# Kernel optimization log

Measured on AMD Instinct MI355X. Metric: run time of the kernel, lower is better.

## Reference

```python
import jax, jax.numpy as jnp
import numpy as np

B, L, DM, DI, N = 8, 2048, 512, 768, 8  # batch, seq, d_model, d_inner=int(1.5*512), d_state


def setup_inputs() -> dict:
    key = jax.random.key(0)
    ks = jax.random.split(key, 8)
    g = lambda k, shape, sc=1.0: (jax.random.normal(k, shape, jnp.float32) * sc)
    return {
        "x": g(ks[0], (B, L, DM)),
        "W_in": g(ks[1], (DM, 2 * DI), 0.02),    # in_proj weight (stored in->out)
        "A_log": g(ks[2], (DI, N)),               # nn.Parameter(randn)
        "D_param": g(ks[3], (DI,)),               # skip-connection D
        "W_x": g(ks[4], (DI, N), 0.02),           # x_proj weight
        "W_dt": g(ks[5], (N, DI), 0.02),          # dt_proj weight
        "b_dt": jnp.zeros((DI,), jnp.float32),    # dt_proj bias
        "W_out": g(ks[6], (DI, DM), 0.02),        # out_proj weight
    }


def reference(x, W_in, A_log, D_param, W_x, W_dt, b_dt, W_out):
    xz = x @ W_in                                  # (B,L,2*DI)
    d_inner = W_in.shape[1] // 2
    x_ssm, z = xz[..., :d_inner], xz[..., d_inner:]
    x_ssm = jax.nn.silu(x_ssm)                     # (B,L,DI)
    A = -jnp.exp(A_log.astype(jnp.float32))        # (DI,N)
    delta = jax.nn.softplus((x_ssm @ W_x) @ W_dt + b_dt)  # (B,L,DI)

    n_state = A.shape[-1]

    def step(h, inp):
        xt, dt = inp                               # each (B,DI)
        dA = jnp.exp(dt[..., None] * A)            # (B,DI,N)
        h = dA * h + dt[..., None] * xt[..., None]
        y = jnp.sum(h, axis=-1) + D_param * xt     # (B,DI)
        return h, y

    h0 = jnp.zeros((x.shape[0], d_inner, n_state), x_ssm.dtype)
    xs = (jnp.swapaxes(x_ssm, 0, 1), jnp.swapaxes(delta, 0, 1))  # (L,B,DI)
    _, ys = jax.lax.scan(step, h0, xs)             # ys: (L,B,DI)
    y = jnp.swapaxes(ys, 0, 1)                     # (B,L,DI)
    y = y * jax.nn.silu(z)
    return y @ W_out                               # (B,L,DM)
```

## Files before the change

### kernel.cpp

```cpp
#include <hip/hip_runtime.h>

typedef unsigned short bfu;
typedef __attribute__((ext_vector_type(8))) short short8;
typedef __attribute__((ext_vector_type(4))) float f32x4;

__device__ __forceinline__ float bf2f(bfu u){
  union { unsigned int i; float f; } v; v.i = ((unsigned int)u) << 16; return v.f;
}
__device__ __forceinline__ bfu f2bf(float f){
  union { float f; unsigned int i; } v; v.f = f;
  unsigned int r = (v.i + 0x7FFFu + ((v.i >> 16) & 1u)) >> 16;
  return (bfu)r;
}
__device__ __forceinline__ float fexp2(float x){ return __builtin_amdgcn_exp2f(x); }
__device__ __forceinline__ float flog2(float x){ return __builtin_amdgcn_logf(x); }
__device__ __forceinline__ float softplusf(float x){
  float t = fexp2(-fabsf(x) * 1.44269504088896f);
  return fmaxf(x, 0.f) + 0.69314718055995f * flog2(1.f + t);
}
__device__ __forceinline__ void gload16(const bfu* g, bfu* l){
  __builtin_amdgcn_global_load_lds((const __attribute__((address_space(1))) unsigned int*)g,
                                   (__attribute__((address_space(3))) unsigned int*)l, 16, 0, 0);
}

__global__ __launch_bounds__(256) void cvt_all_kernel(const float* __restrict__ x, bfu* __restrict__ x_bf,
                                                      const float* __restrict__ W_in, const float* __restrict__ W_out,
                                                      const float* __restrict__ W_x,
                                                      bfu* __restrict__ WinT, bfu* __restrict__ WoutT,
                                                      float* __restrict__ WxT){
  int g = blockIdx.x * 256 + threadIdx.x;
  if (g < 2097152){
    float4 v = ((const float4*)x)[g];
    ushort4 o;
    o.x = f2bf(v.x); o.y = f2bf(v.y); o.z = f2bf(v.z); o.w = f2bf(v.w);
    ((ushort4*)x_bf)[g] = o;
    return;
  }
  int h = g - 2097152;
  if (h < 786432){
    int r = h % 512, c = h / 512;
    WinT[h] = f2bf(W_in[(size_t)r * 1536 + c]);
  } else if (h < 786432 + 393216){
    int h2 = h - 786432;
    int r = h2 % 768, c = h2 / 768;
    WoutT[h2] = f2bf(W_out[(size_t)r * 512 + c]);
  } else if (h < 786432 + 393216 + 6144){
    int h2 = h - (786432 + 393216);
    int n = h2 / 768, k = h2 % 768;
    WxT[h2] = W_x[(size_t)k * 8 + n];
  }
}

template<int EPI, int KK>
__global__ __launch_bounds__(256)
void gemm_db(const bfu* __restrict__ Amat, const bfu* __restrict__ Bt,
             void* __restrict__ out0, void* __restrict__ out1,
             int NBN, int N)
{
  constexpr int NT = KK / 64;
  __shared__ bfu As[2 * 128 * 64];
  __shared__ bfu Bs[2 * 128 * 64];
  const int tid  = threadIdx.x;
  const int lane = tid & 63;
  const int w    = tid >> 6;
  const int wr   = w >> 1, wc = w & 1;

  const int cpx = gridDim.x >> 3;
  const int id  = blockIdx.x;
  const int nid = (id & 7) * cpx + (id >> 3);
  const int bn  = nid % NBN;
  const int bm  = nid / NBN;

  const int srow = tid >> 3;
  const int scol = ((tid & 7) ^ (srow & 7)) * 8;
  const bfu* gA = Amat + ((size_t)(bm * 128 + srow)) * KK + scol;
  const bfu* gB = Bt   + ((size_t)(bn * 128 + srow)) * KK + scol;
  bfu* lA = As + tid * 8;
  bfu* lB = Bs + tid * 8;

  auto STAGE = [&](int t, int sel){
    const int k0 = t * 64;
    #pragma unroll
    for (int i = 0; i < 4; i++){
      gload16(gA + (size_t)(i * 32) * KK + k0, lA + sel * 8192 + i * 2048);
      gload16(gB + (size_t)(i * 32) * KK + k0, lB + sel * 8192 + i * 2048);
    }
  };

  f32x4 acc[4][4];
  #pragma unroll
  for (int i = 0; i < 4; i++)
    #pragma unroll
    for (int j = 0; j < 4; j++)
      #pragma unroll
      for (int r = 0; r < 4; r++) acc[i][j][r] = 0.f;

  STAGE(0, 0);
  STAGE(1, 1);

  #pragma unroll
  for (int t = 0; t < NT; ++t){
    if (t + 1 < NT) asm volatile("s_waitcnt vmcnt(8)" ::: "memory");
    else            asm volatile("s_waitcnt vmcnt(0)" ::: "memory");
    __builtin_amdgcn_s_barrier();

    const bfu* Ab = As + (t & 1) * 8192;
    const bfu* Bb = Bs + (t & 1) * 8192;
    #pragma unroll
    for (int kk = 0; kk < 2; kk++){
      short8 a[4], b[4];
      const int sA = ((kk * 4 + (lane >> 4)) ^ (lane & 7)) * 8;
      #pragma unroll
      for (int m = 0; m < 4; m++){
        int r = wr * 64 + m * 16 + (lane & 15);
        a[m] = *(const short8*)&Ab[r * 64 + sA];
      }
      #pragma unroll
      for (int n = 0; n < 4; n++){
        int r = wc * 64 + n * 16 + (lane & 15);
        b[n] = *(const short8*)&Bb[r * 64 + sA];
      }
      __builtin_amdgcn_s_setprio(1);
      #pragma unroll
      for (int m = 0; m < 4; m++)
        #pragma unroll
        for (int n = 0; n < 4; n++)
          acc[m][n] = __builtin_amdgcn_mfma_f32_16x16x32_bf16(a[m], b[n], acc[m][n], 0, 0, 0);
      __builtin_amdgcn_s_setprio(0);
    }
    __builtin_amdgcn_s_barrier();
    if (t + 2 < NT) STAGE(t + 2, t & 1);
  }

  #pragma unroll
  for (int m = 0; m < 4; m++){
    #pragma unroll
    for (int n = 0; n < 4; n++){
      const int row0 = bm * 128 + wr * 64 + m * 16 + (lane >> 4) * 4;
      const int col  = bn * 128 + wc * 64 + n * 16 + (lane & 15);
      #pragma unroll
      for (int r = 0; r < 4; r++){
        float v = acc[m][n][r];
        int row = row0 + r;
        if (EPI == 0){
          float s = v / (1.f + __expf(-v));
          if (col < 768) ((bfu*)out0)[(size_t)row * 768 + col]         = f2bf(s);
          else           ((bfu*)out1)[(size_t)row * 768 + (col - 768)] = f2bf(s);
        } else {
          ((float*)out0)[(size_t)row * N + col] = v;
        }
      }
    }
  }
}

__global__ __launch_bounds__(256) void u_kernel(const bfu* __restrict__ xssm, const float* __restrict__ WxT,
                                                float* __restrict__ u){
  int wid = threadIdx.x >> 6, lane = threadIdx.x & 63;
  int row = blockIdx.x * 4 + wid;
  const bfu* xr = xssm + (size_t)row * 768;
  float acc[8];
  #pragma unroll
  for (int n = 0; n < 8; n++) acc[n] = 0.f;
  #pragma unroll
  for (int i = 0; i < 3; i++){
    int kb = i * 256 + lane * 4;
    ushort4 xq = *(const ushort4*)(xr + kb);
    float x0 = bf2f(xq.x), x1 = bf2f(xq.y), x2 = bf2f(xq.z), x3 = bf2f(xq.w);
    #pragma unroll
    for (int n = 0; n < 8; n++){
      float4 wv = *(const float4*)(WxT + (size_t)n * 768 + kb);
      acc[n] += x0 * wv.x + x1 * wv.y + x2 * wv.z + x3 * wv.w;
    }
  }
  #pragma unroll
  for (int n = 0; n < 8; n++){
    #pragma unroll
    for (int off = 32; off >= 1; off >>= 1) acc[n] += __shfl_xor(acc[n], off, 64);
  }
  if (lane == 0){
    float4 o0 = { acc[0], acc[1], acc[2], acc[3] };
    float4 o1 = { acc[4], acc[5], acc[6], acc[7] };
    *(float4*)(u + (size_t)row * 8)     = o0;
    *(float4*)(u + (size_t)row * 8 + 4) = o1;
  }
}

__global__ __launch_bounds__(128) void scan_phase1(const bfu* __restrict__ xssm, const float* __restrict__ u,
    const float* __restrict__ Wdt, const float* __restrict__ bdt, const float* __restrict__ A_log,
    float* __restrict__ Pws, float* __restrict__ Hws){
  int tid = threadIdx.x;
  int bid = blockIdx.x;
  int b = bid / 192; int rem = bid % 192;
  int c = rem / 3;   int dblk = rem % 3;
  int d0 = dblk * 256 + tid * 2;
  float Al2[2][8], H[2][8], Wr[2][8], bd[2], S[2];
  #pragma unroll
  for (int j = 0; j < 2; j++){
    bd[j] = bdt[d0 + j];
    S[j] = 0.f;
    #pragma unroll
    for (int n = 0; n < 8; n++){
      Al2[j][n] = -__expf(A_log[(size_t)(d0 + j) * 8 + n]) * 1.4426950408889634f;
      Wr[j][n]  = Wdt[(size_t)n * 768 + d0 + j];
      H[j][n] = 0.f;
    }
  }
  int r0 = b * 2048 + c * 32;
  size_t base = (size_t)r0 * 768 + d0;
  #pragma unroll 8
  for (int i = 0; i < 32; i++){
    float4 u0 = *(const float4*)(u + (size_t)(r0 + i) * 8);
    float4 u1 = *(const float4*)(u + (size_t)(r0 + i) * 8 + 4);
    ushort2 xq = *(const ushort2*)(xssm + base + (size_t)i * 768);
    #pragma unroll
    for (int j = 0; j < 2; j++){
      float xt = bf2f(j == 0 ? xq.x : xq.y);
      float dv = bd[j] + u0.x * Wr[j][0] + u0.y * Wr[j][1] + u0.z * Wr[j][2] + u0.w * Wr[j][3]
                       + u1.x * Wr[j][4] + u1.y * Wr[j][5] + u1.z * Wr[j][6] + u1.w * Wr[j][7];
      float dt = softplusf(dv);
      float dx = dt * xt;
      S[j] += dt;
      #pragma unroll
      for (int n = 0; n < 8; n++){
        float e = fexp2(dt * Al2[j][n]);
        H[j][n] = e * H[j][n] + dx;
      }
    }
  }
  size_t o = (((size_t)b * 64 + c) * 768 + d0) * 8;
  #pragma unroll
  for (int j = 0; j < 2; j++){
    float4 p0, p1;
    p0.x = fexp2(S[j] * Al2[j][0]); p0.y = fexp2(S[j] * Al2[j][1]);
    p0.z = fexp2(S[j] * Al2[j][2]); p0.w = fexp2(S[j] * Al2[j][3]);
    p1.x = fexp2(S[j] * Al2[j][4]); p1.y = fexp2(S[j] * Al2[j][5]);
    p1.z = fexp2(S[j] * Al2[j][6]); p1.w = fexp2(S[j] * Al2[j][7]);
    float4 h0 = { H[j][0], H[j][1], H[j][2], H[j][3] };
    float4 h1 = { H[j][4], H[j][5], H[j][6], H[j][7] };
    *(float4*)(Pws + o + j * 8)     = p0;
    *(float4*)(Pws + o + j * 8 + 4) = p1;
    *(float4*)(Hws + o + j * 8)     = h0;
    *(float4*)(Hws + o + j * 8 + 4) = h1;
  }
}

__global__ __launch_bounds__(256) void scan_phase2(float* __restrict__ Pws, const float* __restrict__ Hws){
  int g = blockIdx.x * 256 + threadIdx.x;
  int within = g % 6144;
  int b = g / 6144;
  size_t base = (size_t)b * 64 * 6144 + within;
  float hin = 0.f;
  #pragma unroll 8
  for (int c = 0; c < 64; c++){
    size_t idx = base + (size_t)c * 6144;
    float p = Pws[idx], hh = Hws[idx];
    Pws[idx] = hin;
    hin = p * hin + hh;
  }
}

__global__ __launch_bounds__(128) void scan_phase3(const bfu* __restrict__ xssm, const float* __restrict__ u,
    const float* __restrict__ Wdt, const float* __restrict__ bdt, const float* __restrict__ A_log,
    const float* __restrict__ Dp, const bfu* __restrict__ siluz, const float* __restrict__ Hin,
    bfu* __restrict__ yz){
  int tid = threadIdx.x;
  int bid = blockIdx.x;
  int b = bid / 192; int rem = bid % 192;
  int c = rem / 3;   int dblk = rem % 3;
  int d0 = dblk * 256 + tid * 2;
  float Al2[2][8], H[2][8], Wr[2][8], bd[2], Dd[2];
  size_t o = (((size_t)b * 64 + c) * 768 + d0) * 8;
  #pragma unroll
  for (int j = 0; j < 2; j++){
    bd[j] = bdt[d0 + j];
    Dd[j] = Dp[d0 + j];
    float4 h0 = *(const float4*)(Hin + o + j * 8);
    float4 h1 = *(const float4*)(Hin + o + j * 8 + 4);
    H[j][0] = h0.x; H[j][1] = h0.y; H[j][2] = h0.z; H[j][3] = h0.w;
    H[j][4] = h1.x; H[j][5] = h1.y; H[j][6] = h1.z; H[j][7] = h1.w;
    #pragma unroll
    for (int n = 0; n < 8; n++){
      Al2[j][n] = -__expf(A_log[(size_t)(d0 + j) * 8 + n]) * 1.4426950408889634f;
      Wr[j][n]  = Wdt[(size_t)n * 768 + d0 + j];
    }
  }
  int r0 = b * 2048 + c * 32;
  size_t base = (size_t)r0 * 768 + d0;
  #pragma unroll 8
  for (int i = 0; i < 32; i++){
    float4 u0 = *(const float4*)(u + (size_t)(r0 + i) * 8);
    float4 u1 = *(const float4*)(u + (size_t)(r0 + i) * 8 + 4);
    ushort2 xq = *(const ushort2*)(xssm + base + (size_t)i * 768);
    ushort2 zq = *(const ushort2*)(siluz + base + (size_t)i * 768);
    ushort2 oq;
    #pragma unroll
    for (int j = 0; j < 2; j++){
      float xt = bf2f(j == 0 ? xq.x : xq.y);
      float dv = bd[j] + u0.x * Wr[j][0] + u0.y * Wr[j][1] + u0.z * Wr[j][2] + u0.w * Wr[j][3]
                       + u1.x * Wr[j][4] + u1.y * Wr[j][5] + u1.z * Wr[j][6] + u1.w * Wr[j][7];
      float dt = softplusf(dv);
      float dx = dt * xt;
      float y = Dd[j] * xt;
      #pragma unroll
      for (int n = 0; n < 8; n++){
        float e = fexp2(dt * Al2[j][n]);
        H[j][n] = e * H[j][n] + dx;
        y += H[j][n];
      }
      float sz = bf2f(j == 0 ? zq.x : zq.y);
      bfu r = f2bf(y * sz);
      if (j == 0) oq.x = r; else oq.y = r;
    }
    *(ushort2*)(yz + base + (size_t)i * 768) = oq;
  }
}

extern "C" void kernel_launch(void* const* d_in, const int* in_sizes, int n_in,
                              void* d_out, int out_size, void* d_ws, size_t ws_size,
                              hipStream_t stream){
  const float* x     = (const float*)d_in[0];
  const float* W_in  = (const float*)d_in[1];
  const float* A_log = (const float*)d_in[2];
  const float* D_par = (const float*)d_in[3];
  const float* W_x   = (const float*)d_in[4];
  const float* W_dt  = (const float*)d_in[5];
  const float* b_dt  = (const float*)d_in[6];
  const float* W_out = (const float*)d_in[7];
  float* out = (float*)d_out;
  (void)in_sizes; (void)n_in; (void)out_size; (void)ws_size;

  char* base = (char*)d_ws;
  size_t off = 0;
  auto alloc = [&](size_t bytes)->char*{
    char* p = base + off; off += (bytes + 255) & ~(size_t)255; return p;
  };
  bfu*   x_bf  = (bfu*)  alloc((size_t)16384 * 512 * 2);
  bfu*   WinT  = (bfu*)  alloc((size_t)1536 * 512 * 2);
  bfu*   WoutT = (bfu*)  alloc((size_t)512 * 768 * 2);
  float* WxT   = (float*)alloc((size_t)8 * 768 * 4);
  bfu*   xssm  = (bfu*)  alloc((size_t)16384 * 768 * 2);
  bfu*   siluz = (bfu*)  alloc((size_t)16384 * 768 * 2);
  float* u     = (float*)alloc((size_t)16384 * 8 * 4);
  float* Pws   = (float*)alloc((size_t)8 * 64 * 768 * 8 * 4);
  float* Hws   = (float*)alloc((size_t)8 * 64 * 768 * 8 * 4);
  bfu*   yz    = (bfu*)  alloc((size_t)16384 * 768 * 2);

  cvt_all_kernel<<<12824, 256, 0, stream>>>(x, x_bf, W_in, W_out, W_x, WinT, WoutT, WxT);
  gemm_db<0, 512><<<1536, 256, 0, stream>>>(x_bf, WinT, xssm, siluz, 12, 1536);
  u_kernel<<<4096, 256, 0, stream>>>(xssm, WxT, u);
  scan_phase1<<<1536, 128, 0, stream>>>(xssm, u, W_dt, b_dt, A_log, Pws, Hws);
  scan_phase2<<<192, 256, 0, stream>>>(Pws, Hws);
  scan_phase3<<<1536, 128, 0, stream>>>(xssm, u, W_dt, b_dt, A_log, D_par, siluz, Pws, yz);
  gemm_db<1, 768><<<512, 256, 0, stream>>>(yz, WoutT, out, nullptr, 4, 512);
}
```

Baseline: 168.5 us.

## Use triple-buffered 128x256 GEMM tiles with 512 threads and interleaved LDS loads

Both projection GEMMs move from a 128x128 double-buffered tile with 4 waves to a 128x256 tile with 8 waves and three LDS stages. The next-next stage is issued right after the barrier, so the trailing barrier goes away, and LDS fragment loads are interleaved with MFMA groups. The aim is to hide global-load latency better, drop one barrier per k-step, and reuse each A tile across more output columns. In exchange, LDS use per block rises to 144KB, which limits residency to one block per CU, and the grids become smaller (768 and 256 blocks).

```diff
diff --git a/kernel.cpp b/kernel.cpp
--- a/kernel.cpp
+++ b/kernel.cpp
@@ -52,18 +52,17 @@
 }
 
 template<int EPI, int KK>
-__global__ __launch_bounds__(256)
-void gemm_db(const bfu* __restrict__ Amat, const bfu* __restrict__ Bt,
+__global__ __launch_bounds__(512)
+void gemm_3s(const bfu* __restrict__ Amat, const bfu* __restrict__ Bt,
              void* __restrict__ out0, void* __restrict__ out1,
              int NBN, int N)
 {
   constexpr int NT = KK / 64;
-  __shared__ bfu As[2 * 128 * 64];
-  __shared__ bfu Bs[2 * 128 * 64];
+  __shared__ bfu LDS[3 * 24576];
   const int tid  = threadIdx.x;
   const int lane = tid & 63;
   const int w    = tid >> 6;
-  const int wr   = w >> 1, wc = w & 1;
+  const int wr   = w >> 2, wc = w & 3;
 
   const int cpx = gridDim.x >> 3;
   const int id  = blockIdx.x;
@@ -74,17 +73,17 @@
   const int srow = tid >> 3;
   const int scol = ((tid & 7) ^ (srow & 7)) * 8;
   const bfu* gA = Amat + ((size_t)(bm * 128 + srow)) * KK + scol;
-  const bfu* gB = Bt   + ((size_t)(bn * 128 + srow)) * KK + scol;
-  bfu* lA = As + tid * 8;
-  bfu* lB = Bs + tid * 8;
-
-  auto STAGE = [&](int t, int sel){
+  const bfu* gB = Bt   + ((size_t)(bn * 256 + srow)) * KK + scol;
+
+  auto STAGE = [&](int t, int buf){
     const int k0 = t * 64;
-    #pragma unroll
-    for (int i = 0; i < 4; i++){
-      gload16(gA + (size_t)(i * 32) * KK + k0, lA + sel * 8192 + i * 2048);
-      gload16(gB + (size_t)(i * 32) * KK + k0, lB + sel * 8192 + i * 2048);
-    }
+    bfu* dst = LDS + buf * 24576 + tid * 8;
+    #pragma unroll
+    for (int i = 0; i < 2; i++)
+      gload16(gA + (size_t)(i * 64) * KK + k0, dst + i * 4096);
+    #pragma unroll
+    for (int j = 0; j < 4; j++)
+      gload16(gB + (size_t)(j * 64) * KK + k0, dst + 8192 + j * 4096);
   };
 
   f32x4 acc[4][4];
@@ -100,36 +99,49 @@
 
   #pragma unroll
   for (int t = 0; t < NT; ++t){
-    if (t + 1 < NT) asm volatile("s_waitcnt vmcnt(8)" ::: "memory");
+    if (t + 1 < NT) asm volatile("s_waitcnt vmcnt(6)" ::: "memory");
     else            asm volatile("s_waitcnt vmcnt(0)" ::: "memory");
     __builtin_amdgcn_s_barrier();
 
-    const bfu* Ab = As + (t & 1) * 8192;
-    const bfu* Bb = Bs + (t & 1) * 8192;
-    #pragma unroll
-    for (int kk = 0; kk < 2; kk++){
-      short8 a[4], b[4];
-      const int sA = ((kk * 4 + (lane >> 4)) ^ (lane & 7)) * 8;
-      #pragma unroll
-      for (int m = 0; m < 4; m++){
-        int r = wr * 64 + m * 16 + (lane & 15);
-        a[m] = *(const short8*)&Ab[r * 64 + sA];
-      }
-      #pragma unroll
-      for (int n = 0; n < 4; n++){
-        int r = wc * 64 + n * 16 + (lane & 15);
-        b[n] = *(const short8*)&Bb[r * 64 + sA];
-      }
-      __builtin_amdgcn_s_setprio(1);
-      #pragma unroll
-      for (int m = 0; m < 4; m++)
-        #pragma unroll
-        for (int n = 0; n < 4; n++)
-          acc[m][n] = __builtin_amdgcn_mfma_f32_16x16x32_bf16(a[m], b[n], acc[m][n], 0, 0, 0);
+    if (t + 2 < NT) STAGE(t + 2, (t + 2) % 3);
+
+    const bfu* Ab = LDS + (t % 3) * 24576;
+    const bfu* Bb = Ab + 8192;
+    short8 a[2][2], b[4][2];
+
+    #define LDA(mh)                                                             \
+      _Pragma("unroll") for (int mi = 0; mi < 2; mi++)                          \
+      _Pragma("unroll") for (int kk = 0; kk < 2; kk++){                         \
+        int r_ = wr * 64 + ((mh) * 2 + mi) * 16 + (lane & 15);                  \
+        int s_ = (kk * 4 + (lane >> 4)) ^ (r_ & 7);                             \
+        a[mi][kk] = *(const short8*)&Ab[r_ * 64 + s_ * 8];                      \
+      }
+    #define LDB(nh)                                                             \
+      _Pragma("unroll") for (int ni = 0; ni < 2; ni++)                          \
+      _Pragma("unroll") for (int kk = 0; kk < 2; kk++){                         \
+        int r_ = wc * 64 + ((nh) * 2 + ni) * 16 + (lane & 15);                  \
+        int s_ = (kk * 4 + (lane >> 4)) ^ (r_ & 7);                             \
+        b[(nh) * 2 + ni][kk] = *(const short8*)&Bb[r_ * 64 + s_ * 8];           \
+      }
+    #define MFMA8(mh, nh)                                                       \
+      __builtin_amdgcn_s_setprio(1);                                            \
+      _Pragma("unroll") for (int mi = 0; mi < 2; mi++)                          \
+      _Pragma("unroll") for (int ni = 0; ni < 2; ni++)                          \
+      _Pragma("unroll") for (int kk = 0; kk < 2; kk++)                          \
+        acc[(mh)*2+mi][(nh)*2+ni] = __builtin_amdgcn_mfma_f32_16x16x32_bf16(    \
+            a[mi][kk], b[(nh)*2+ni][kk], acc[(mh)*2+mi][(nh)*2+ni], 0, 0, 0);   \
       __builtin_amdgcn_s_setprio(0);
-    }
-    __builtin_amdgcn_s_barrier();
-    if (t + 2 < NT) STAGE(t + 2, t & 1);
+
+    LDA(0); LDB(0);
+    MFMA8(0, 0);
+    LDB(1);
+    MFMA8(0, 1);
+    LDA(1);
+    MFMA8(1, 0);
+    MFMA8(1, 1);
+    #undef LDA
+    #undef LDB
+    #undef MFMA8
   }
 
   #pragma unroll
@@ -137,7 +149,7 @@
     #pragma unroll
     for (int n = 0; n < 4; n++){
       const int row0 = bm * 128 + wr * 64 + m * 16 + (lane >> 4) * 4;
-      const int col  = bn * 128 + wc * 64 + n * 16 + (lane & 15);
+      const int col  = bn * 256 + wc * 64 + n * 16 + (lane & 15);
       #pragma unroll
       for (int r = 0; r < 4; r++){
         float v = acc[m][n][r];
@@ -347,10 +359,10 @@
   bfu*   yz    = (bfu*)  alloc((size_t)16384 * 768 * 2);
 
   cvt_all_kernel<<<12824, 256, 0, stream>>>(x, x_bf, W_in, W_out, W_x, WinT, WoutT, WxT);
-  gemm_db<0, 512><<<1536, 256, 0, stream>>>(x_bf, WinT, xssm, siluz, 12, 1536);
+  gemm_3s<0, 512><<<768, 512, 0, stream>>>(x_bf, WinT, xssm, siluz, 6, 1536);
   u_kernel<<<4096, 256, 0, stream>>>(xssm, WxT, u);
   scan_phase1<<<1536, 128, 0, stream>>>(xssm, u, W_dt, b_dt, A_log, Pws, Hws);
   scan_phase2<<<192, 256, 0, stream>>>(Pws, Hws);
   scan_phase3<<<1536, 128, 0, stream>>>(xssm, u, W_dt, b_dt, A_log, D_par, siluz, Pws, yz);
-  gemm_db<1, 768><<<512, 256, 0, stream>>>(yz, WoutT, out, nullptr, 4, 512);
-}
+  gemm_3s<1, 768><<<256, 512, 0, stream>>>(yz, WoutT, out, nullptr, 2, 512);
+}
```

Result: no change. 166.1 us (-1.4%).

## Rewrite GEMM as 256x128 tile with triple-buffered LDS and split-phase loads

Applied to the files above, without the earlier changes.

The GEMM kernel now computes a 256x128 output tile per block (8x4 MFMA tiles per wave) with a K step of 32, using a three-stage LDS ring buffer. Global-to-LDS loads for A and B are issued in separate phases interleaved with the two halves of the MFMA work, and a new rotation swizzle replaces the XOR layout. The aim is more reuse per loaded byte and better overlap of memory with compute. The cost is twice the accumulator registers per thread, half the grid size (which may leave CUs underfilled for the out-projection), and more barriers per iteration.

```diff
diff --git a/kernel.cpp b/kernel.cpp
--- a/kernel.cpp
+++ b/kernel.cpp
@@ -53,13 +53,12 @@
 
 template<int EPI, int KK>
 __global__ __launch_bounds__(256)
-void gemm_db(const bfu* __restrict__ Amat, const bfu* __restrict__ Bt,
+void gemm_8p(const bfu* __restrict__ Amat, const bfu* __restrict__ Bt,
              void* __restrict__ out0, void* __restrict__ out1,
              int NBN, int N)
 {
-  constexpr int NT = KK / 64;
-  __shared__ bfu As[2 * 128 * 64];
-  __shared__ bfu Bs[2 * 128 * 64];
+  constexpr int NT = KK / 32;
+  __shared__ bfu LDS[3 * 12288];
   const int tid  = threadIdx.x;
   const int lane = tid & 63;
   const int w    = tid >> 6;
@@ -71,72 +70,99 @@
   const int bn  = nid % NBN;
   const int bm  = nid / NBN;
 
-  const int srow = tid >> 3;
-  const int scol = ((tid & 7) ^ (srow & 7)) * 8;
-  const bfu* gA = Amat + ((size_t)(bm * 128 + srow)) * KK + scol;
-  const bfu* gB = Bt   + ((size_t)(bn * 128 + srow)) * KK + scol;
-  bfu* lA = As + tid * 8;
-  bfu* lB = Bs + tid * 8;
-
-  auto STAGE = [&](int t, int sel){
-    const int k0 = t * 64;
-    #pragma unroll
-    for (int i = 0; i < 4; i++){
-      gload16(gA + (size_t)(i * 32) * KK + k0, lA + sel * 8192 + i * 2048);
-      gload16(gB + (size_t)(i * 32) * KK + k0, lB + sel * 8192 + i * 2048);
-    }
+  const int grow  = tid >> 2;
+  const int gslot = ((tid & 3) - ((tid >> 3) & 3)) & 3;
+  const bfu* gA = Amat + ((size_t)(bm * 256 + grow)) * KK + gslot * 8;
+  const bfu* gB = Bt   + ((size_t)(bn * 128 + grow)) * KK + gslot * 8;
+
+  auto STAGE_A = [&](int t, int buf){
+    const int k0 = t * 32;
+    bfu* dst = (bfu*)LDS + buf * 12288 + tid * 8;
+    #pragma unroll
+    for (int i = 0; i < 4; i++)
+      gload16(gA + (size_t)(i * 64) * KK + k0, dst + i * 2048);
   };
-
-  f32x4 acc[4][4];
-  #pragma unroll
-  for (int i = 0; i < 4; i++)
+  auto STAGE_B = [&](int t, int buf){
+    const int k0 = t * 32;
+    bfu* dst = (bfu*)LDS + buf * 12288 + 8192 + tid * 8;
+    #pragma unroll
+    for (int j = 0; j < 2; j++)
+      gload16(gB + (size_t)(j * 64) * KK + k0, dst + j * 2048);
+  };
+
+  const int rslot = (((lane >> 4) + ((lane & 15) >> 1)) & 3) * 8;
+  const int aoff  = (wr * 128 + (lane & 15)) * 32 + rslot;
+  const int boff  = 8192 + (wc * 64 + (lane & 15)) * 32 + rslot;
+
+  f32x4 acc[8][4];
+  #pragma unroll
+  for (int i = 0; i < 8; i++)
     #pragma unroll
     for (int j = 0; j < 4; j++)
       #pragma unroll
       for (int r = 0; r < 4; r++) acc[i][j][r] = 0.f;
 
-  STAGE(0, 0);
-  STAGE(1, 1);
-
-  #pragma unroll
+  STAGE_A(0, 0); STAGE_B(0, 0);
+  STAGE_A(1, 1); STAGE_B(1, 1);
+  asm volatile("s_waitcnt vmcnt(6)" ::: "memory");
+  __builtin_amdgcn_s_barrier();
+
+  int cur = 0, s2 = 2;
   for (int t = 0; t < NT; ++t){
-    if (t + 1 < NT) asm volatile("s_waitcnt vmcnt(8)" ::: "memory");
-    else            asm volatile("s_waitcnt vmcnt(0)" ::: "memory");
+    const bfu* Lb = (const bfu*)LDS + cur * 12288;
+    short8 a0, a1, a2, a3, b0, b1, b2, b3;
+
+    a0 = *(const short8*)&Lb[aoff + 0 * 512];
+    a1 = *(const short8*)&Lb[aoff + 1 * 512];
+    a2 = *(const short8*)&Lb[aoff + 2 * 512];
+    a3 = *(const short8*)&Lb[aoff + 3 * 512];
+    b0 = *(const short8*)&Lb[boff + 0 * 512];
+    b1 = *(const short8*)&Lb[boff + 1 * 512];
+    b2 = *(const short8*)&Lb[boff + 2 * 512];
+    b3 = *(const short8*)&Lb[boff + 3 * 512];
+    if (t + 2 < NT) STAGE_A(t + 2, s2);
     __builtin_amdgcn_s_barrier();
-
-    const bfu* Ab = As + (t & 1) * 8192;
-    const bfu* Bb = Bs + (t & 1) * 8192;
-    #pragma unroll
-    for (int kk = 0; kk < 2; kk++){
-      short8 a[4], b[4];
-      const int sA = ((kk * 4 + (lane >> 4)) ^ (lane & 7)) * 8;
-      #pragma unroll
-      for (int m = 0; m < 4; m++){
-        int r = wr * 64 + m * 16 + (lane & 15);
-        a[m] = *(const short8*)&Ab[r * 64 + sA];
-      }
-      #pragma unroll
-      for (int n = 0; n < 4; n++){
-        int r = wc * 64 + n * 16 + (lane & 15);
-        b[n] = *(const short8*)&Bb[r * 64 + sA];
-      }
-      __builtin_amdgcn_s_setprio(1);
-      #pragma unroll
-      for (int m = 0; m < 4; m++)
-        #pragma unroll
-        for (int n = 0; n < 4; n++)
-          acc[m][n] = __builtin_amdgcn_mfma_f32_16x16x32_bf16(a[m], b[n], acc[m][n], 0, 0, 0);
-      __builtin_amdgcn_s_setprio(0);
-    }
+    __builtin_amdgcn_s_setprio(1);
+    #pragma unroll
+    for (int mi = 0; mi < 4; mi++){
+      const short8 am = (mi == 0) ? a0 : (mi == 1) ? a1 : (mi == 2) ? a2 : a3;
+      acc[mi][0] = __builtin_amdgcn_mfma_f32_16x16x32_bf16(am, b0, acc[mi][0], 0, 0, 0);
+      acc[mi][1] = __builtin_amdgcn_mfma_f32_16x16x32_bf16(am, b1, acc[mi][1], 0, 0, 0);
+      acc[mi][2] = __builtin_amdgcn_mfma_f32_16x16x32_bf16(am, b2, acc[mi][2], 0, 0, 0);
+      acc[mi][3] = __builtin_amdgcn_mfma_f32_16x16x32_bf16(am, b3, acc[mi][3], 0, 0, 0);
+    }
+    __builtin_amdgcn_s_setprio(0);
     __builtin_amdgcn_s_barrier();
-    if (t + 2 < NT) STAGE(t + 2, t & 1);
-  }
-
-  #pragma unroll
-  for (int m = 0; m < 4; m++){
+
+    a0 = *(const short8*)&Lb[aoff + 4 * 512];
+    a1 = *(const short8*)&Lb[aoff + 5 * 512];
+    a2 = *(const short8*)&Lb[aoff + 6 * 512];
+    a3 = *(const short8*)&Lb[aoff + 7 * 512];
+    if (t + 2 < NT) STAGE_B(t + 2, s2);
+    __builtin_amdgcn_s_barrier();
+    __builtin_amdgcn_s_setprio(1);
+    #pragma unroll
+    for (int mi = 0; mi < 4; mi++){
+      const short8 am = (mi == 0) ? a0 : (mi == 1) ? a1 : (mi == 2) ? a2 : a3;
+      acc[4 + mi][0] = __builtin_amdgcn_mfma_f32_16x16x32_bf16(am, b0, acc[4 + mi][0], 0, 0, 0);
+      acc[4 + mi][1] = __builtin_amdgcn_mfma_f32_16x16x32_bf16(am, b1, acc[4 + mi][1], 0, 0, 0);
+      acc[4 + mi][2] = __builtin_amdgcn_mfma_f32_16x16x32_bf16(am, b2, acc[4 + mi][2], 0, 0, 0);
+      acc[4 + mi][3] = __builtin_amdgcn_mfma_f32_16x16x32_bf16(am, b3, acc[4 + mi][3], 0, 0, 0);
+    }
+    __builtin_amdgcn_s_setprio(0);
+    __builtin_amdgcn_s_barrier();
+
+    if (t < NT - 2)       asm volatile("s_waitcnt vmcnt(6)" ::: "memory");
+    else if (t == NT - 2) asm volatile("s_waitcnt vmcnt(0)" ::: "memory");
+    cur = (cur == 2) ? 0 : cur + 1;
+    s2  = (s2  == 2) ? 0 : s2  + 1;
+  }
+
+  #pragma unroll
+  for (int m = 0; m < 8; m++){
     #pragma unroll
     for (int n = 0; n < 4; n++){
-      const int row0 = bm * 128 + wr * 64 + m * 16 + (lane >> 4) * 4;
+      const int row0 = bm * 256 + wr * 128 + m * 16 + (lane >> 4) * 4;
       const int col  = bn * 128 + wc * 64 + n * 16 + (lane & 15);
       #pragma unroll
       for (int r = 0; r < 4; r++){
@@ -347,10 +373,10 @@
   bfu*   yz    = (bfu*)  alloc((size_t)16384 * 768 * 2);
 
   cvt_all_kernel<<<12824, 256, 0, stream>>>(x, x_bf, W_in, W_out, W_x, WinT, WoutT, WxT);
-  gemm_db<0, 512><<<1536, 256, 0, stream>>>(x_bf, WinT, xssm, siluz, 12, 1536);
+  gemm_8p<0, 512><<<768, 256, 0, stream>>>(x_bf, WinT, xssm, siluz, 12, 1536);
   u_kernel<<<4096, 256, 0, stream>>>(xssm, WxT, u);
   scan_phase1<<<1536, 128, 0, stream>>>(xssm, u, W_dt, b_dt, A_log, Pws, Hws);
   scan_phase2<<<192, 256, 0, stream>>>(Pws, Hws);
   scan_phase3<<<1536, 128, 0, stream>>>(xssm, u, W_dt, b_dt, A_log, D_par, siluz, Pws, yz);
-  gemm_db<1, 768><<<512, 256, 0, stream>>>(yz, WoutT, out, nullptr, 4, 512);
-}
+  gemm_8p<1, 768><<<256, 256, 0, stream>>>(yz, WoutT, out, nullptr, 4, 512);
+}
```

Result: slower. 194.5 us (+15.4%).

## Enlarge GEMM tiles to 256x128 with 8 waves and restructure prefetch pipeline

Applied to the files above, without the earlier changes.

Switches both projection GEMMs to a 512-thread block computing a 256x128 output tile, so each B tile staged in LDS is reused across twice as many rows. The K loop changes from issuing loads two stages ahead with a partial vmcnt wait to prefetching one stage ahead, with a full wait and barrier after each compute step. The larger tile halves the grid and raises LDS use per block, which may lower occupancy. The fuller wait may also expose more global-load latency.

```diff
diff --git a/kernel.cpp b/kernel.cpp
--- a/kernel.cpp
+++ b/kernel.cpp
@@ -52,14 +52,13 @@
 }
 
 template<int EPI, int KK>
-__global__ __launch_bounds__(256)
-void gemm_db(const bfu* __restrict__ Amat, const bfu* __restrict__ Bt,
+__global__ __launch_bounds__(512)
+void gemm_2p(const bfu* __restrict__ Amat, const bfu* __restrict__ Bt,
              void* __restrict__ out0, void* __restrict__ out1,
              int NBN, int N)
 {
   constexpr int NT = KK / 64;
-  __shared__ bfu As[2 * 128 * 64];
-  __shared__ bfu Bs[2 * 128 * 64];
+  __shared__ bfu LDS[2 * 24576];
   const int tid  = threadIdx.x;
   const int lane = tid & 63;
   const int w    = tid >> 6;
@@ -73,18 +72,18 @@
 
   const int srow = tid >> 3;
   const int scol = ((tid & 7) ^ (srow & 7)) * 8;
-  const bfu* gA = Amat + ((size_t)(bm * 128 + srow)) * KK + scol;
+  const bfu* gA = Amat + ((size_t)(bm * 256 + srow)) * KK + scol;
   const bfu* gB = Bt   + ((size_t)(bn * 128 + srow)) * KK + scol;
-  bfu* lA = As + tid * 8;
-  bfu* lB = Bs + tid * 8;
-
-  auto STAGE = [&](int t, int sel){
+
+  auto STAGE = [&](int t, int buf){
     const int k0 = t * 64;
-    #pragma unroll
-    for (int i = 0; i < 4; i++){
-      gload16(gA + (size_t)(i * 32) * KK + k0, lA + sel * 8192 + i * 2048);
-      gload16(gB + (size_t)(i * 32) * KK + k0, lB + sel * 8192 + i * 2048);
-    }
+    bfu* dst = (bfu*)LDS + buf * 24576 + tid * 8;
+    #pragma unroll
+    for (int i = 0; i < 4; i++)
+      gload16(gA + (size_t)(i * 64) * KK + k0, dst + i * 4096);
+    #pragma unroll
+    for (int j = 0; j < 2; j++)
+      gload16(gB + (size_t)(j * 64) * KK + k0, dst + 16384 + j * 4096);
   };
 
   f32x4 acc[4][4];
@@ -96,16 +95,15 @@
       for (int r = 0; r < 4; r++) acc[i][j][r] = 0.f;
 
   STAGE(0, 0);
-  STAGE(1, 1);
-
-  #pragma unroll
+  asm volatile("s_waitcnt vmcnt(0)" ::: "memory");
+  __builtin_amdgcn_s_barrier();
+
+  int cur = 0;
   for (int t = 0; t < NT; ++t){
-    if (t + 1 < NT) asm volatile("s_waitcnt vmcnt(8)" ::: "memory");
-    else            asm volatile("s_waitcnt vmcnt(0)" ::: "memory");
-    __builtin_amdgcn_s_barrier();
-
-    const bfu* Ab = As + (t & 1) * 8192;
-    const bfu* Bb = Bs + (t & 1) * 8192;
+    if (t + 1 < NT) STAGE(t + 1, cur ^ 1);
+
+    const bfu* Ab = (const bfu*)LDS + cur * 24576;
+    const bfu* Bb = Ab + 16384;
     #pragma unroll
     for (int kk = 0; kk < 2; kk++){
       short8 a[4], b[4];
@@ -128,15 +126,19 @@
           acc[m][n] = __builtin_amdgcn_mfma_f32_16x16x32_bf16(a[m], b[n], acc[m][n], 0, 0, 0);
       __builtin_amdgcn_s_setprio(0);
     }
-    __builtin_amdgcn_s_barrier();
-    if (t + 2 < NT) STAGE(t + 2, t & 1);
+
+    if (t + 1 < NT){
+      asm volatile("s_waitcnt vmcnt(0)" ::: "memory");
+      __builtin_amdgcn_s_barrier();
+      cur ^= 1;
+    }
   }
 
   #pragma unroll
   for (int m = 0; m < 4; m++){
     #pragma unroll
     for (int n = 0; n < 4; n++){
-      const int row0 = bm * 128 + wr * 64 + m * 16 + (lane >> 4) * 4;
+      const int row0 = bm * 256 + wr * 64 + m * 16 + (lane >> 4) * 4;
       const int col  = bn * 128 + wc * 64 + n * 16 + (lane & 15);
       #pragma unroll
       for (int r = 0; r < 4; r++){
@@ -347,10 +349,10 @@
   bfu*   yz    = (bfu*)  alloc((size_t)16384 * 768 * 2);
 
   cvt_all_kernel<<<12824, 256, 0, stream>>>(x, x_bf, W_in, W_out, W_x, WinT, WoutT, WxT);
-  gemm_db<0, 512><<<1536, 256, 0, stream>>>(x_bf, WinT, xssm, siluz, 12, 1536);
+  gemm_2p<0, 512><<<768, 512, 0, stream>>>(x_bf, WinT, xssm, siluz, 12, 1536);
   u_kernel<<<4096, 256, 0, stream>>>(xssm, WxT, u);
   scan_phase1<<<1536, 128, 0, stream>>>(xssm, u, W_dt, b_dt, A_log, Pws, Hws);
   scan_phase2<<<192, 256, 0, stream>>>(Pws, Hws);
   scan_phase3<<<1536, 128, 0, stream>>>(xssm, u, W_dt, b_dt, A_log, D_par, siluz, Pws, yz);
-  gemm_db<1, 768><<<512, 256, 0, stream>>>(yz, WoutT, out, nullptr, 4, 512);
-}
+  gemm_2p<1, 768><<<256, 512, 0, stream>>>(yz, WoutT, out, nullptr, 4, 512);
+}
```

Result: no change. 165.8 us (-1.6%).
